# Kernel optimization log

Hardware: AMD Instinct MI355X
Metric: run time of the kernel (lower is better)

## Reference

```python
import jax, jax.numpy as jnp
import numpy as np

B, NC, NT = 16, 2048, 2048
IN_DIM, H_DIM, OUT_DIM = 128, 256, 256


def _mlp(x, w1, b1, w2, b2, w3, b3):
    # MLP(input_dim, [h, h], output_dim): Linear-ReLU-Linear-ReLU-Linear
    h = jax.nn.relu(x @ w1 + b1)
    h = jax.nn.relu(h @ w2 + b2)
    return h @ w3 + b3


def setup_inputs() -> dict:
    key = jax.random.key(0)
    ks = jax.random.split(key, 16)

    def lin(k, fan_in, fan_out):
        s = 1.0 / np.sqrt(fan_in)
        kw, kb = jax.random.split(k)
        w = jax.random.uniform(kw, (fan_in, fan_out), jnp.float32, -s, s)
        b = jax.random.uniform(kb, (fan_out,), jnp.float32, -s, s)
        return w, b

    qw1, qb1 = lin(ks[0], IN_DIM, H_DIM)
    qw2, qb2 = lin(ks[1], H_DIM, H_DIM)
    qw3, qb3 = lin(ks[2], H_DIM, OUT_DIM)
    kw1, kb1 = lin(ks[3], IN_DIM, H_DIM)
    kw2, kb2 = lin(ks[4], H_DIM, H_DIM)
    kw3, kb3 = lin(ks[5], H_DIM, OUT_DIM)

    return {
        "x_context": jax.random.normal(ks[6], (B, NC, IN_DIM), jnp.float32),
        "x_target": jax.random.normal(ks[7], (B, NT, IN_DIM), jnp.float32),
        "r_i": jax.random.normal(ks[8], (B, NC, OUT_DIM), jnp.float32),
        "qw1": qw1, "qb1": qb1, "qw2": qw2, "qb2": qb2, "qw3": qw3, "qb3": qb3,
        "kw1": kw1, "kb1": kb1, "kw2": kw2, "kb2": kb2, "kw3": kw3, "kb3": kb3,
    }


def reference(x_context, x_target, r_i,
              qw1, qb1, qw2, qb2, qw3, qb3,
              kw1, kb1, kw2, kb2, kw3, kb3):
    q = _mlp(x_target, qw1, qb1, qw2, qb2, qw3, qb3)   # [B, NT, D]
    k = _mlp(x_context, kw1, kb1, kw2, kb2, kw3, kb3)  # [B, NC, D]
    scale = jnp.sqrt(jnp.asarray(k.shape[-1], dtype=jnp.float32))
    w = jnp.einsum('btd,bcd->btc', q, k) / scale       # [B, NT, NC]
    # Faithful to torch.softmax(w, dim=1): normalize over the TARGET axis.
    w = jax.nn.softmax(w, axis=1)
    return jnp.einsum('btc,bcd->btd', w, r_i)          # [B, NT, OUT_DIM]
```

## Files before the change

kernel.cpp:

```cpp
#include <hip/hip_runtime.h>

#define BB 16
#define NT 2048
#define NC 2048
#define DIM 256
#define INDIM 128

typedef unsigned short u16;
typedef __bf16 bfx8 __attribute__((ext_vector_type(8)));
typedef __bf16 bfx8a __attribute__((ext_vector_type(8), aligned(8)));
typedef float f32x4 __attribute__((ext_vector_type(4)));

__device__ __forceinline__ u16 f2bf(float f) {
    union { float f; unsigned u; } v; v.f = f;
    return (u16)((v.u + 0x7FFFu + ((v.u >> 16) & 1u)) >> 16);
}

#define MFMA16(a, b, c) __builtin_amdgcn_mfma_f32_16x16x32_bf16((a), (b), (c), 0, 0, 0)


__global__ void cvt_w_all(const float* __restrict__ w0, const float* __restrict__ w1,
                          const float* __restrict__ w2, const float* __restrict__ w3,
                          const float* __restrict__ w4, const float* __restrict__ w5,
                          u16* __restrict__ o0, u16* __restrict__ o1, u16* __restrict__ o2,
                          u16* __restrict__ o3, u16* __restrict__ o4, u16* __restrict__ o5) {
    int bx = blockIdx.x;
    const float* src; u16* dst; int K, base;
    if (bx < 128)       { src = w0; dst = o0; K = 128; base = 0; }
    else if (bx < 384)  { src = w1; dst = o1; K = 256; base = 128; }
    else if (bx < 640)  { src = w2; dst = o2; K = 256; base = 384; }
    else if (bx < 768)  { src = w3; dst = o3; K = 128; base = 640; }
    else if (bx < 1024) { src = w4; dst = o4; K = 256; base = 768; }
    else                { src = w5; dst = o5; K = 256; base = 1024; }
    int idx = (bx - base) * 256 + threadIdx.x;
    int n = idx / K, k = idx - n * K;
    dst[idx] = f2bf(src[k * 256 + n]);
}

__global__ __launch_bounds__(256) void cvt_rt_kernel(const float* __restrict__ r, u16* __restrict__ rt) {
    __shared__ u16 t[64][68];
    int b = blockIdx.z;
    int c0 = blockIdx.x * 64, d0 = blockIdx.y * 64;
    int tid = threadIdx.x;
    const float* rb = r + (size_t)b * NC * DIM + d0;
    int cr = tid >> 4, df = (tid & 15) * 4;
#pragma unroll
    for (int p = 0; p < 4; p++) {
        int c = p * 16 + cr;
        float4 v = *reinterpret_cast<const float4*>(rb + (size_t)(c0 + c) * DIM + df);
        t[df + 0][c] = f2bf(v.x);
        t[df + 1][c] = f2bf(v.y);
        t[df + 2][c] = f2bf(v.z);
        t[df + 3][c] = f2bf(v.w);
    }
    __syncthreads();
    u16* rtb = rt + (size_t)b * DIM * NC;
    int dr = tid >> 3, cc = (tid & 7) * 8;
#pragma unroll
    for (int p = 0; p < 2; p++) {
        int d = p * 32 + dr;
        union { u16 u[8]; uint4 v; } pk;
#pragma unroll
        for (int j = 0; j < 8; j++) pk.u[j] = t[d][cc + j];
        *reinterpret_cast<uint4*>(rtb + (size_t)(d0 + d) * NC + c0 + cc) = pk.v;
    }
}


__global__ __launch_bounds__(256) void mlp_fused(const float* __restrict__ xq, const float* __restrict__ xk,
                                                 const u16* __restrict__ W1q, const u16* __restrict__ W1k,
                                                 const float* __restrict__ b1q, const float* __restrict__ b1k,
                                                 const u16* __restrict__ W2q, const u16* __restrict__ W2k,
                                                 const float* __restrict__ b2q, const float* __restrict__ b2k,
                                                 const u16* __restrict__ W3q, const u16* __restrict__ W3k,
                                                 const float* __restrict__ b3q, const float* __restrict__ b3k,
                                                 u16* __restrict__ oq, u16* __restrict__ ok) {
    __shared__ __align__(16) char lds[65536];
    char* h1 = lds;
    char* xa = lds + 32768;
    char* h2 = lds + 32768;

    int tid = threadIdx.x, lane = tid & 63, w = tid >> 6;
    int lr = lane & 15, lg = lane >> 4;
    int m0 = blockIdx.x * 64;
    bool isq = (blockIdx.y == 0);
    const float* X = (isq ? xq : xk) + (size_t)m0 * INDIM;
    const u16* W1 = isq ? W1q : W1k;  const float* b1 = isq ? b1q : b1k;
    const u16* W2 = isq ? W2q : W2k;  const float* b2 = isq ? b2q : b2k;
    const u16* W3 = isq ? W3q : W3k;  const float* b3 = isq ? b3q : b3k;
    u16* C = (isq ? oq : ok) + (size_t)m0 * 256;

#pragma unroll
    for (int j = 0; j < 4; j++) {
        int bo = (j * 256 + tid) * 16;
        int row = bo >> 8;
        int ir = bo & 255;
        const float* src = X + (size_t)row * INDIM + (ir >> 1);
        float4 f0 = *reinterpret_cast<const float4*>(src);
        float4 f1 = *reinterpret_cast<const float4*>(src + 4);
        union { u16 u[8]; uint4 v; } pk;
        pk.u[0] = f2bf(f0.x); pk.u[1] = f2bf(f0.y); pk.u[2] = f2bf(f0.z); pk.u[3] = f2bf(f0.w);
        pk.u[4] = f2bf(f1.x); pk.u[5] = f2bf(f1.y); pk.u[6] = f2bf(f1.z); pk.u[7] = f2bf(f1.w);
        *reinterpret_cast<uint4*>(xa + row * 256 + (ir ^ ((row & 7) << 4))) = pk.v;
    }
    __syncthreads();

    int n0 = w * 64;
    const int key = (lr & 7) << 4;

    {
        f32x4 acc[4][4] = {};
#pragma unroll
        for (int ks = 0; ks < 4; ks++) {
            bfx8 b[4];
#pragma unroll
            for (int nt = 0; nt < 4; nt++)
                b[nt] = *reinterpret_cast<const bfx8*>(W1 + (size_t)(n0 + nt * 16 + lr) * 128 + ks * 32 + lg * 8);
#pragma unroll
            for (int mt = 0; mt < 4; mt++) {
                bfx8 a = *reinterpret_cast<const bfx8*>(xa + (mt * 16 + lr) * 256 + ((ks * 64 + lg * 16) ^ key));
#pragma unroll
                for (int nt = 0; nt < 4; nt++)
                    acc[mt][nt] = MFMA16(a, b[nt], acc[mt][nt]);
            }
        }
#pragma unroll
        for (int nt = 0; nt < 4; nt++) {
            int col = n0 + nt * 16 + lr;
            float bv = b1[col];
#pragma unroll
            for (int mt = 0; mt < 4; mt++) {
#pragma unroll
                for (int r = 0; r < 4; r++) {
                    int row = mt * 16 + lg * 4 + r;
                    float v = fmaxf(acc[mt][nt][r] + bv, 0.0f);
                    *(u16*)(h1 + row * 512 + ((col * 2) ^ ((row & 7) << 4))) = f2bf(v);
                }
            }
        }
    }
    __syncthreads();

    {
        f32x4 acc[4][4] = {};
#pragma unroll
        for (int ks = 0; ks < 8; ks++) {
            bfx8 b[4];
#pragma unroll
            for (int nt = 0; nt < 4; nt++)
                b[nt] = *reinterpret_cast<const bfx8*>(W2 + (size_t)(n0 + nt * 16 + lr) * 256 + ks * 32 + lg * 8);
#pragma unroll
            for (int mt = 0; mt < 4; mt++) {
                bfx8 a = *reinterpret_cast<const bfx8*>(h1 + (mt * 16 + lr) * 512 + ((ks * 64 + lg * 16) ^ key));
#pragma unroll
                for (int nt = 0; nt < 4; nt++)
                    acc[mt][nt] = MFMA16(a, b[nt], acc[mt][nt]);
            }
        }
#pragma unroll
        for (int nt = 0; nt < 4; nt++) {
            int col = n0 + nt * 16 + lr;
            float bv = b2[col];
#pragma unroll
            for (int mt = 0; mt < 4; mt++) {
#pragma unroll
                for (int r = 0; r < 4; r++) {
                    int row = mt * 16 + lg * 4 + r;
                    float v = fmaxf(acc[mt][nt][r] + bv, 0.0f);
                    *(u16*)(h2 + row * 512 + ((col * 2) ^ ((row & 7) << 4))) = f2bf(v);
                }
            }
        }
    }
    __syncthreads();

    {
        f32x4 acc[4][4] = {};
#pragma unroll
        for (int ks = 0; ks < 8; ks++) {
            bfx8 b[4];
#pragma unroll
            for (int nt = 0; nt < 4; nt++)
                b[nt] = *reinterpret_cast<const bfx8*>(W3 + (size_t)(n0 + nt * 16 + lr) * 256 + ks * 32 + lg * 8);
#pragma unroll
            for (int mt = 0; mt < 4; mt++) {
                bfx8 a = *reinterpret_cast<const bfx8*>(h2 + (mt * 16 + lr) * 512 + ((ks * 64 + lg * 16) ^ key));
#pragma unroll
                for (int nt = 0; nt < 4; nt++)
                    acc[mt][nt] = MFMA16(a, b[nt], acc[mt][nt]);
            }
        }
        u16* ot = (u16*)h1;
#pragma unroll
        for (int nt = 0; nt < 4; nt++) {
            int col = n0 + nt * 16 + lr;
            float bv = b3[col];
#pragma unroll
            for (int mt = 0; mt < 4; mt++) {
#pragma unroll
                for (int r = 0; r < 4; r++) {
                    int row = mt * 16 + lg * 4 + r;
                    ot[row * 256 + col] = f2bf(acc[mt][nt][r] + bv);
                }
            }
        }
        __syncthreads();
#pragma unroll
        for (int p = 0; p < 8; p++) {
            int idx = p * 256 + tid;
            int row = idx >> 5, ck = idx & 31;
            *reinterpret_cast<uint4*>(C + (size_t)row * 256 + ck * 8) =
                *reinterpret_cast<const uint4*>(ot + row * 256 + ck * 8);
        }
    }
}


__global__ __launch_bounds__(256) void stats_kernel(const u16* __restrict__ q,
                                                    const u16* __restrict__ k,
                                                    float2* __restrict__ gso) {
    int flat = blockIdx.x;
    int sw = (flat & 7) * 64 + (flat >> 3);
    int b = sw >> 5;
    int c0 = (sw & 31) * 64;
    int tid = threadIdx.x, lane = tid & 63, w = tid >> 6;
    int lr = lane & 15, lg = lane >> 4;
    const u16* qb = q + (size_t)b * NT * DIM;
    const u16* kb = k + (size_t)b * NC * DIM;
    const float A2 = 1.44269504f / 16.0f;

    bfx8 kf[4][8];
#pragma unroll
    for (int j = 0; j < 4; j++)
#pragma unroll
        for (int ks = 0; ks < 8; ks++)
            kf[j][ks] = *reinterpret_cast<const bfx8*>(kb + (size_t)(c0 + j * 16 + lr) * DIM + ks * 32 + lg * 8);

    float m_run[4], l_run[4];
#pragma unroll
    for (int j = 0; j < 4; j++) { m_run[j] = -1e30f; l_run[j] = 0.0f; }

#define LOADQ(dst, ts_) do {                                                        \
    const u16* qrow_ = qb + (size_t)((ts_) * 64 + w * 16 + lr) * DIM;               \
    _Pragma("unroll")                                                               \
    for (int ks_ = 0; ks_ < 8; ks_++)                                               \
        dst[ks_] = *reinterpret_cast<const bfx8*>(qrow_ + ks_ * 32 + lg * 8);       \
} while (0)

#define STEP(aq_) do {                                                              \
    f32x4 sacc[4] = {};                                                             \
    _Pragma("unroll")                                                               \
    for (int ks_ = 0; ks_ < 8; ks_++) {                                             \
        _Pragma("unroll")                                                           \
        for (int j_ = 0; j_ < 4; j_++)                                              \
            sacc[j_] = MFMA16(aq_[ks_], kf[j_][ks_], sacc[j_]);                     \
    }                                                                               \
    _Pragma("unroll")                                                               \
    for (int j_ = 0; j_ < 4; j_++) {                                                \
        f32x4 a_ = sacc[j_];                                                        \
        float mx_ = fmaxf(fmaxf(a_[0], a_[1]), fmaxf(a_[2], a_[3]));                \
        if (mx_ > m_run[j_] + 88.0f) {                                              \
            l_run[j_] *= exp2f((m_run[j_] - mx_) * A2);                             \
            m_run[j_] = mx_;                                                        \
        }                                                                           \
        float t_ = m_run[j_] * A2;                                                  \
        l_run[j_] += exp2f(fmaf(a_[0], A2, -t_)) + exp2f(fmaf(a_[1], A2, -t_))      \
                   + exp2f(fmaf(a_[2], A2, -t_)) + exp2f(fmaf(a_[3], A2, -t_));     \
    }                                                                               \
} while (0)

    bfx8 a0[8], a1[8];
    LOADQ(a0, 0);
    for (int ts = 0; ts < NT / 64; ts += 2) {
        LOADQ(a1, ts + 1);
        STEP(a0);
        if (ts + 2 < NT / 64) LOADQ(a0, ts + 2);
        STEP(a1);
    }
#undef LOADQ
#undef STEP

#pragma unroll
    for (int j = 0; j < 4; j++) {
        float m = m_run[j], l = l_run[j];
#pragma unroll
        for (int d = 16; d < 64; d <<= 1) {
            float mo = __shfl_xor(m, d);
            float lo = __shfl_xor(l, d);
            float mn = fmaxf(m, mo);
            l = l * exp2f((m - mn) * A2) + lo * exp2f((mo - mn) * A2);
            m = mn;
        }
        m_run[j] = m; l_run[j] = l;
    }

    __shared__ float sm[4][64], sl[4][64];
    if (lg == 0) {
#pragma unroll
        for (int j = 0; j < 4; j++) {
            sm[w][j * 16 + lr] = m_run[j];
            sl[w][j * 16 + lr] = l_run[j];
        }
    }
    __syncthreads();
    if (tid < 64) {
        float mf = sm[0][tid];
#pragma unroll
        for (int ww = 1; ww < 4; ww++) mf = fmaxf(mf, sm[ww][tid]);
        float lf = 0.0f;
#pragma unroll
        for (int ww = 0; ww < 4; ww++) lf += sl[ww][tid] * exp2f((sm[ww][tid] - mf) * A2);
        gso[(size_t)b * NC + c0 + tid] = make_float2(mf * A2, 1.0f / lf);
    }
}


__global__ __launch_bounds__(256, 2) void attn_kernel(const u16* __restrict__ q,
                                                      const u16* __restrict__ k,
                                                      const u16* __restrict__ rt,
                                                      const float2* __restrict__ gsg_,
                                                      float* __restrict__ out) {
    int flat = blockIdx.x;
    int sw = (flat & 7) * 64 + (flat >> 3);
    int b = sw >> 5;
    int t0 = (sw & 31) * 64;
    int tid = threadIdx.x, lane = tid & 63, w = tid >> 6;
    int lr = lane & 15, lg = lane >> 4;
    const u16* qb = q + (size_t)b * NT * DIM;
    const u16* kb = k + (size_t)b * NC * DIM;
    const u16* rtb = rt + (size_t)b * DIM * NC;

    __shared__ float2 gs[NC];
    __shared__ __align__(16) u16 kt[2][32 * 256];
    __shared__ u16 pl[64][36];

    {
        const float2* gsg = gsg_ + (size_t)b * NC;
        for (int i = tid; i < NC; i += 256) gs[i] = gsg[i];
    }
    __syncthreads();

#define STAGE(nb, cc) do {                                                          \
    const u16* ksrc_ = kb + (size_t)(cc) * DIM;                                     \
    _Pragma("unroll")                                                               \
    for (int i_ = 0; i_ < 4; i_++) {                                                \
        int off_ = ((w * 4 + i_) << 10) + (lane << 4);                              \
        int row_ = off_ >> 9;                                                       \
        int ss_  = ((off_ >> 4) & 31) ^ (row_ & 7);                                 \
        const u16* g_ = ksrc_ + row_ * DIM + ss_ * 8;                               \
        __builtin_amdgcn_global_load_lds(                                           \
            (const __attribute__((address_space(1))) void*)g_,                      \
            (__attribute__((address_space(3))) void*)(&kt[nb][(w * 4 + i_) << 9]),  \
            16, 0, 0);                                                              \
    }                                                                               \
} while (0)

    STAGE(0, 0);
    __builtin_amdgcn_sched_barrier(0);
    bfx8 rb_c[4], rb_n[4];
#pragma unroll
    for (int nt = 0; nt < 4; nt++)
        rb_c[nt] = *reinterpret_cast<const bfx8*>(rtb + (size_t)(w * 64 + nt * 16 + lr) * NC + lg * 8);
    bfx8 aq[8];
#pragma unroll
    for (int ks = 0; ks < 8; ks++)
        aq[ks] = *reinterpret_cast<const bfx8*>(qb + (size_t)(t0 + w * 16 + lr) * DIM + ks * 32 + lg * 8);
    __builtin_amdgcn_sched_barrier(0);
    asm volatile("s_waitcnt vmcnt(12)");
    __builtin_amdgcn_s_barrier();
    __builtin_amdgcn_sched_barrier(0);

    const float A = 1.44269504f / 16.0f;
    const int key = lr & 7;
    f32x4 acc[4][4] = {};
    int cur = 0;

    for (int c0 = 0; c0 < NC; c0 += 32) {
        const bool last = (c0 + 32 >= NC);
        if (!last) STAGE(cur ^ 1, c0 + 32);
        __builtin_amdgcn_sched_barrier(0);
        if (!last) {
#pragma unroll
            for (int nt = 0; nt < 4; nt++)
                rb_n[nt] = *reinterpret_cast<const bfx8*>(rtb + (size_t)(w * 64 + nt * 16 + lr) * NC + (c0 + 32) + lg * 8);
        }

        f32x4 s[2] = {};
        {
            const char* kc = (const char*)&kt[cur][0];
#pragma unroll
            for (int ks = 0; ks < 8; ks++) {
                int slot = (ks << 2) | lg;
                bfx8 k0 = *reinterpret_cast<const bfx8*>(kc + (lr << 9) + (((slot ^ key)) << 4));
                bfx8 k1 = *reinterpret_cast<const bfx8*>(kc + ((16 + lr) << 9) + (((slot ^ key)) << 4));
                s[0] = MFMA16(aq[ks], k0, s[0]);
                s[1] = MFMA16(aq[ks], k1, s[1]);
            }
        }
#pragma unroll
        for (int j = 0; j < 2; j++) {
            float2 g = gs[c0 + j * 16 + lr];
#pragma unroll
            for (int r = 0; r < 4; r++) {
                float p = exp2f(fmaf(s[j][r], A, -g.x)) * g.y;
                __bf16 h = (__bf16)p;
                pl[w * 16 + lg * 4 + r][j * 16 + lr] = *(u16*)&h;
            }
        }
        __builtin_amdgcn_sched_barrier(0);
        asm volatile("s_waitcnt lgkmcnt(0)");
        __builtin_amdgcn_s_barrier();
        __builtin_amdgcn_sched_barrier(0);

#pragma unroll
        for (int mt = 0; mt < 4; mt++) {
            bfx8a pa = *reinterpret_cast<const bfx8a*>((const char*)pl + (mt * 16 + lr) * 72 + lg * 16);
#pragma unroll
            for (int nt = 0; nt < 4; nt++)
                acc[mt][nt] = MFMA16((bfx8)pa, rb_c[nt], acc[mt][nt]);
        }

        __builtin_amdgcn_sched_barrier(0);
        asm volatile("s_waitcnt vmcnt(4) lgkmcnt(0)");
        __builtin_amdgcn_s_barrier();
        __builtin_amdgcn_sched_barrier(0);

#pragma unroll
        for (int nt = 0; nt < 4; nt++) rb_c[nt] = rb_n[nt];
        cur ^= 1;
    }
#undef STAGE

    float* ob = out + (size_t)b * NT * DIM;
#pragma unroll
    for (int nt = 0; nt < 4; nt++) {
        int col = w * 64 + nt * 16 + lr;
#pragma unroll
        for (int mt = 0; mt < 4; mt++) {
            int rowb = t0 + mt * 16 + lg * 4;
#pragma unroll
            for (int r = 0; r < 4; r++)
                ob[(size_t)(rowb + r) * DIM + col] = acc[mt][nt][r];
        }
    }
}


extern "C" void kernel_launch(void* const* d_in, const int* in_sizes, int n_in,
                              void* d_out, int out_size, void* d_ws, size_t ws_size,
                              hipStream_t stream) {
    const float* xc  = (const float*)d_in[0];
    const float* xt  = (const float*)d_in[1];
    const float* ri  = (const float*)d_in[2];
    const float* qw1 = (const float*)d_in[3];  const float* qb1 = (const float*)d_in[4];
    const float* qw2 = (const float*)d_in[5];  const float* qb2 = (const float*)d_in[6];
    const float* qw3 = (const float*)d_in[7];  const float* qb3 = (const float*)d_in[8];
    const float* kw1 = (const float*)d_in[9];  const float* kb1 = (const float*)d_in[10];
    const float* kw2 = (const float*)d_in[11]; const float* kb2 = (const float*)d_in[12];
    const float* kw3 = (const float*)d_in[13]; const float* kb3 = (const float*)d_in[14];

    if (ws_size < ((size_t)66 << 20)) return;

    char* ws = (char*)d_ws;
    u16* q   = (u16*)(ws);
    u16* kk  = (u16*)(ws + ((size_t)16 << 20));
    u16* rt  = (u16*)(ws + ((size_t)32 << 20));
    float2* gsb = (float2*)(ws + ((size_t)48 << 20));
    u16* wbuf = (u16*)(ws + ((size_t)48 << 20) + (512 << 10));
    u16* qw1t = wbuf;
    u16* qw2t = qw1t + 32768;
    u16* qw3t = qw2t + 65536;
    u16* kw1t = qw3t + 65536;
    u16* kw2t = kw1t + 32768;
    u16* kw3t = kw2t + 65536;

    cvt_w_all<<<dim3(1280), 256, 0, stream>>>(qw1, qw2, qw3, kw1, kw2, kw3,
                                              qw1t, qw2t, qw3t, kw1t, kw2t, kw3t);

    mlp_fused<<<dim3(512, 2), 256, 0, stream>>>(xt, xc,
                                                qw1t, kw1t, qb1, kb1,
                                                qw2t, kw2t, qb2, kb2,
                                                qw3t, kw3t, qb3, kb3,
                                                q, kk);

    cvt_rt_kernel<<<dim3(32, 4, BB), 256, 0, stream>>>(ri, rt);

    stats_kernel<<<dim3(512), 256, 0, stream>>>(q, kk, gsb);

    attn_kernel<<<dim3(512), 256, 0, stream>>>(q, kk, rt, gsb, (float*)d_out);
}
```

Measured before the change: 251.4 us.

## Halve MLP row tile and merge r transpose into stats kernel launch

The MLP kernel now processes 32 rows per block instead of 64, which halves LDS use and doubles the grid so more blocks can be resident and the work is spread more evenly. The r_i transpose/convert kernel is folded into the stats kernel as extra blocks (indices 512 and up), removing one launch and letting the bandwidth-bound conversion run alongside the compute-bound stats pass. The cost is that each MLP block reuses the weights it loads across fewer rows, and the stats blocks share a kernel with different register and LDS needs.

Result: slower. 271.1 us (+7.9%).

```diff
diff --git a/kernel.cpp b/kernel.cpp
--- a/kernel.cpp
+++ b/kernel.cpp
@@ -37,35 +37,6 @@
     dst[idx] = f2bf(src[k * 256 + n]);
 }
 
-__global__ __launch_bounds__(256) void cvt_rt_kernel(const float* __restrict__ r, u16* __restrict__ rt) {
-    __shared__ u16 t[64][68];
-    int b = blockIdx.z;
-    int c0 = blockIdx.x * 64, d0 = blockIdx.y * 64;
-    int tid = threadIdx.x;
-    const float* rb = r + (size_t)b * NC * DIM + d0;
-    int cr = tid >> 4, df = (tid & 15) * 4;
-#pragma unroll
-    for (int p = 0; p < 4; p++) {
-        int c = p * 16 + cr;
-        float4 v = *reinterpret_cast<const float4*>(rb + (size_t)(c0 + c) * DIM + df);
-        t[df + 0][c] = f2bf(v.x);
-        t[df + 1][c] = f2bf(v.y);
-        t[df + 2][c] = f2bf(v.z);
-        t[df + 3][c] = f2bf(v.w);
-    }
-    __syncthreads();
-    u16* rtb = rt + (size_t)b * DIM * NC;
-    int dr = tid >> 3, cc = (tid & 7) * 8;
-#pragma unroll
-    for (int p = 0; p < 2; p++) {
-        int d = p * 32 + dr;
-        union { u16 u[8]; uint4 v; } pk;
-#pragma unroll
-        for (int j = 0; j < 8; j++) pk.u[j] = t[d][cc + j];
-        *reinterpret_cast<uint4*>(rtb + (size_t)(d0 + d) * NC + c0 + cc) = pk.v;
-    }
-}
-
 
 __global__ __launch_bounds__(256) void mlp_fused(const float* __restrict__ xq, const float* __restrict__ xk,
                                                  const u16* __restrict__ W1q, const u16* __restrict__ W1k,
@@ -75,14 +46,14 @@
                                                  const u16* __restrict__ W3q, const u16* __restrict__ W3k,
                                                  const float* __restrict__ b3q, const float* __restrict__ b3k,
                                                  u16* __restrict__ oq, u16* __restrict__ ok) {
-    __shared__ __align__(16) char lds[65536];
+    __shared__ __align__(16) char lds[32768];
     char* h1 = lds;
-    char* xa = lds + 32768;
-    char* h2 = lds + 32768;
+    char* xa = lds + 16384;
+    char* h2 = lds + 16384;
 
     int tid = threadIdx.x, lane = tid & 63, w = tid >> 6;
     int lr = lane & 15, lg = lane >> 4;
-    int m0 = blockIdx.x * 64;
+    int m0 = blockIdx.x * 32;
     bool isq = (blockIdx.y == 0);
     const float* X = (isq ? xq : xk) + (size_t)m0 * INDIM;
     const u16* W1 = isq ? W1q : W1k;  const float* b1 = isq ? b1q : b1k;
@@ -91,7 +62,7 @@
     u16* C = (isq ? oq : ok) + (size_t)m0 * 256;
 
 #pragma unroll
-    for (int j = 0; j < 4; j++) {
+    for (int j = 0; j < 2; j++) {
         int bo = (j * 256 + tid) * 16;
         int row = bo >> 8;
         int ir = bo & 255;
@@ -109,7 +80,7 @@
     const int key = (lr & 7) << 4;
 
     {
-        f32x4 acc[4][4] = {};
+        f32x4 acc[2][4] = {};
 #pragma unroll
         for (int ks = 0; ks < 4; ks++) {
             bfx8 b[4];
@@ -117,7 +88,7 @@
             for (int nt = 0; nt < 4; nt++)
                 b[nt] = *reinterpret_cast<const bfx8*>(W1 + (size_t)(n0 + nt * 16 + lr) * 128 + ks * 32 + lg * 8);
 #pragma unroll
-            for (int mt = 0; mt < 4; mt++) {
+            for (int mt = 0; mt < 2; mt++) {
                 bfx8 a = *reinterpret_cast<const bfx8*>(xa + (mt * 16 + lr) * 256 + ((ks * 64 + lg * 16) ^ key));
 #pragma unroll
                 for (int nt = 0; nt < 4; nt++)
@@ -129,7 +100,7 @@
             int col = n0 + nt * 16 + lr;
             float bv = b1[col];
 #pragma unroll
-            for (int mt = 0; mt < 4; mt++) {
+            for (int mt = 0; mt < 2; mt++) {
 #pragma unroll
                 for (int r = 0; r < 4; r++) {
                     int row = mt * 16 + lg * 4 + r;
@@ -142,7 +113,7 @@
     __syncthreads();
 
     {
-        f32x4 acc[4][4] = {};
+        f32x4 acc[2][4] = {};
 #pragma unroll
         for (int ks = 0; ks < 8; ks++) {
             bfx8 b[4];
@@ -150,7 +121,7 @@
             for (int nt = 0; nt < 4; nt++)
                 b[nt] = *reinterpret_cast<const bfx8*>(W2 + (size_t)(n0 + nt * 16 + lr) * 256 + ks * 32 + lg * 8);
 #pragma unroll
-            for (int mt = 0; mt < 4; mt++) {
+            for (int mt = 0; mt < 2; mt++) {
                 bfx8 a = *reinterpret_cast<const bfx8*>(h1 + (mt * 16 + lr) * 512 + ((ks * 64 + lg * 16) ^ key));
 #pragma unroll
                 for (int nt = 0; nt < 4; nt++)
@@ -162,7 +133,7 @@
             int col = n0 + nt * 16 + lr;
             float bv = b2[col];
 #pragma unroll
-            for (int mt = 0; mt < 4; mt++) {
+            for (int mt = 0; mt < 2; mt++) {
 #pragma unroll
                 for (int r = 0; r < 4; r++) {
                     int row = mt * 16 + lg * 4 + r;
@@ -175,7 +146,7 @@
     __syncthreads();
 
     {
-        f32x4 acc[4][4] = {};
+        f32x4 acc[2][4] = {};
 #pragma unroll
         for (int ks = 0; ks < 8; ks++) {
             bfx8 b[4];
@@ -183,7 +154,7 @@
             for (int nt = 0; nt < 4; nt++)
                 b[nt] = *reinterpret_cast<const bfx8*>(W3 + (size_t)(n0 + nt * 16 + lr) * 256 + ks * 32 + lg * 8);
 #pragma unroll
-            for (int mt = 0; mt < 4; mt++) {
+            for (int mt = 0; mt < 2; mt++) {
                 bfx8 a = *reinterpret_cast<const bfx8*>(h2 + (mt * 16 + lr) * 512 + ((ks * 64 + lg * 16) ^ key));
 #pragma unroll
                 for (int nt = 0; nt < 4; nt++)
@@ -196,7 +167,7 @@
             int col = n0 + nt * 16 + lr;
             float bv = b3[col];
 #pragma unroll
-            for (int mt = 0; mt < 4; mt++) {
+            for (int mt = 0; mt < 2; mt++) {
 #pragma unroll
                 for (int r = 0; r < 4; r++) {
                     int row = mt * 16 + lg * 4 + r;
@@ -206,7 +177,7 @@
         }
         __syncthreads();
 #pragma unroll
-        for (int p = 0; p < 8; p++) {
+        for (int p = 0; p < 4; p++) {
             int idx = p * 256 + tid;
             int row = idx >> 5, ck = idx & 31;
             *reinterpret_cast<uint4*>(C + (size_t)row * 256 + ck * 8) =
@@ -216,29 +187,35 @@
 }
 
 
-__global__ __launch_bounds__(256) void stats_kernel(const u16* __restrict__ q,
-                                                    const u16* __restrict__ k,
-                                                    float2* __restrict__ gso) {
-    int flat = blockIdx.x;
-    int sw = (flat & 7) * 64 + (flat >> 3);
-    int b = sw >> 5;
-    int c0 = (sw & 31) * 64;
-    int tid = threadIdx.x, lane = tid & 63, w = tid >> 6;
-    int lr = lane & 15, lg = lane >> 4;
-    const u16* qb = q + (size_t)b * NT * DIM;
-    const u16* kb = k + (size_t)b * NC * DIM;
-    const float A2 = 1.44269504f / 16.0f;
-
-    bfx8 kf[4][8];
-#pragma unroll
-    for (int j = 0; j < 4; j++)
-#pragma unroll
-        for (int ks = 0; ks < 8; ks++)
-            kf[j][ks] = *reinterpret_cast<const bfx8*>(kb + (size_t)(c0 + j * 16 + lr) * DIM + ks * 32 + lg * 8);
-
-    float m_run[4], l_run[4];
-#pragma unroll
-    for (int j = 0; j < 4; j++) { m_run[j] = -1e30f; l_run[j] = 0.0f; }
+__global__ __launch_bounds__(256) void stats_rt_kernel(const u16* __restrict__ q,
+                                                       const u16* __restrict__ k,
+                                                       float2* __restrict__ gso,
+                                                       const float* __restrict__ r,
+                                                       u16* __restrict__ rt) {
+    __shared__ __align__(16) char shmem[64 * 68 * 2];
+
+    int tid = threadIdx.x;
+    if (blockIdx.x < 512) {
+        int flat = blockIdx.x;
+        int sw = (flat & 7) * 64 + (flat >> 3);
+        int b = sw >> 5;
+        int c0 = (sw & 31) * 64;
+        int lane = tid & 63, w = tid >> 6;
+        int lr = lane & 15, lg = lane >> 4;
+        const u16* qb = q + (size_t)b * NT * DIM;
+        const u16* kb = k + (size_t)b * NC * DIM;
+        const float A2 = 1.44269504f / 16.0f;
+
+        bfx8 kf[4][8];
+#pragma unroll
+        for (int j = 0; j < 4; j++)
+#pragma unroll
+            for (int ks = 0; ks < 8; ks++)
+                kf[j][ks] = *reinterpret_cast<const bfx8*>(kb + (size_t)(c0 + j * 16 + lr) * DIM + ks * 32 + lg * 8);
+
+        float m_run[4], l_run[4];
+#pragma unroll
+        for (int j = 0; j < 4; j++) { m_run[j] = -1e30f; l_run[j] = 0.0f; }
 
 #define LOADQ(dst, ts_) do {                                                        \
     const u16* qrow_ = qb + (size_t)((ts_) * 64 + w * 16 + lr) * DIM;               \
@@ -269,48 +246,78 @@
     }                                                                               \
 } while (0)
 
-    bfx8 a0[8], a1[8];
-    LOADQ(a0, 0);
-    for (int ts = 0; ts < NT / 64; ts += 2) {
-        LOADQ(a1, ts + 1);
-        STEP(a0);
-        if (ts + 2 < NT / 64) LOADQ(a0, ts + 2);
-        STEP(a1);
-    }
+        bfx8 a0[8], a1[8];
+        LOADQ(a0, 0);
+        for (int ts = 0; ts < NT / 64; ts += 2) {
+            LOADQ(a1, ts + 1);
+            STEP(a0);
+            if (ts + 2 < NT / 64) LOADQ(a0, ts + 2);
+            STEP(a1);
+        }
 #undef LOADQ
 #undef STEP
 
 #pragma unroll
-    for (int j = 0; j < 4; j++) {
-        float m = m_run[j], l = l_run[j];
-#pragma unroll
-        for (int d = 16; d < 64; d <<= 1) {
-            float mo = __shfl_xor(m, d);
-            float lo = __shfl_xor(l, d);
-            float mn = fmaxf(m, mo);
-            l = l * exp2f((m - mn) * A2) + lo * exp2f((mo - mn) * A2);
-            m = mn;
-        }
-        m_run[j] = m; l_run[j] = l;
-    }
-
-    __shared__ float sm[4][64], sl[4][64];
-    if (lg == 0) {
-#pragma unroll
         for (int j = 0; j < 4; j++) {
-            sm[w][j * 16 + lr] = m_run[j];
-            sl[w][j * 16 + lr] = l_run[j];
-        }
-    }
-    __syncthreads();
-    if (tid < 64) {
-        float mf = sm[0][tid];
-#pragma unroll
-        for (int ww = 1; ww < 4; ww++) mf = fmaxf(mf, sm[ww][tid]);
-        float lf = 0.0f;
-#pragma unroll
-        for (int ww = 0; ww < 4; ww++) lf += sl[ww][tid] * exp2f((sm[ww][tid] - mf) * A2);
-        gso[(size_t)b * NC + c0 + tid] = make_float2(mf * A2, 1.0f / lf);
+            float m = m_run[j], l = l_run[j];
+#pragma unroll
+            for (int d = 16; d < 64; d <<= 1) {
+                float mo = __shfl_xor(m, d);
+                float lo = __shfl_xor(l, d);
+                float mn = fmaxf(m, mo);
+                l = l * exp2f((m - mn) * A2) + lo * exp2f((mo - mn) * A2);
+                m = mn;
+            }
+            m_run[j] = m; l_run[j] = l;
+        }
+
+        float* sm = (float*)shmem;
+        float* sl = sm + 256;
+        if (lg == 0) {
+#pragma unroll
+            for (int j = 0; j < 4; j++) {
+                sm[w * 64 + j * 16 + lr] = m_run[j];
+                sl[w * 64 + j * 16 + lr] = l_run[j];
+            }
+        }
+        __syncthreads();
+        if (tid < 64) {
+            float mf = sm[tid];
+#pragma unroll
+            for (int ww = 1; ww < 4; ww++) mf = fmaxf(mf, sm[ww * 64 + tid]);
+            float lf = 0.0f;
+#pragma unroll
+            for (int ww = 0; ww < 4; ww++) lf += sl[ww * 64 + tid] * exp2f((sm[ww * 64 + tid] - mf) * A2);
+            gso[(size_t)b * NC + c0 + tid] = make_float2(mf * A2, 1.0f / lf);
+        }
+    } else {
+        int idx = blockIdx.x - 512;
+        int b = idx >> 7;
+        int d0 = ((idx >> 5) & 3) * 64;
+        int c0 = (idx & 31) * 64;
+        u16 (*t)[68] = (u16(*)[68])shmem;
+        const float* rb = r + (size_t)b * NC * DIM + d0;
+        int cr = tid >> 4, df = (tid & 15) * 4;
+#pragma unroll
+        for (int p = 0; p < 4; p++) {
+            int c = p * 16 + cr;
+            float4 v = *reinterpret_cast<const float4*>(rb + (size_t)(c0 + c) * DIM + df);
+            t[df + 0][c] = f2bf(v.x);
+            t[df + 1][c] = f2bf(v.y);
+            t[df + 2][c] = f2bf(v.z);
+            t[df + 3][c] = f2bf(v.w);
+        }
+        __syncthreads();
+        u16* rtb = rt + (size_t)b * DIM * NC;
+        int dr = tid >> 3, cc = (tid & 7) * 8;
+#pragma unroll
+        for (int p = 0; p < 2; p++) {
+            int d = p * 32 + dr;
+            union { u16 u[8]; uint4 v; } pk;
+#pragma unroll
+            for (int j = 0; j < 8; j++) pk.u[j] = t[d][cc + j];
+            *reinterpret_cast<uint4*>(rtb + (size_t)(d0 + d) * NC + c0 + cc) = pk.v;
+        }
     }
 }
 
@@ -477,15 +484,13 @@
     cvt_w_all<<<dim3(1280), 256, 0, stream>>>(qw1, qw2, qw3, kw1, kw2, kw3,
                                               qw1t, qw2t, qw3t, kw1t, kw2t, kw3t);
 
-    mlp_fused<<<dim3(512, 2), 256, 0, stream>>>(xt, xc,
-                                                qw1t, kw1t, qb1, kb1,
-                                                qw2t, kw2t, qb2, kb2,
-                                                qw3t, kw3t, qb3, kb3,
-                                                q, kk);
-
-    cvt_rt_kernel<<<dim3(32, 4, BB), 256, 0, stream>>>(ri, rt);
-
-    stats_kernel<<<dim3(512), 256, 0, stream>>>(q, kk, gsb);
+    mlp_fused<<<dim3(1024, 2), 256, 0, stream>>>(xt, xc,
+                                                 qw1t, kw1t, qb1, kb1,
+                                                 qw2t, kw2t, qb2, kb2,
+                                                 qw3t, kw3t, qb3, kb3,
+                                                 q, kk);
+
+    stats_rt_kernel<<<dim3(2560), 256, 0, stream>>>(q, kk, gsb, ri, rt);
 
     attn_kernel<<<dim3(512), 256, 0, stream>>>(q, kk, rt, gsb, (float*)d_out);
 }
```
